# Optimization experiments

Hardware: AMD Instinct MI355X
Metric: run time of the kernel (lower is better)

Reference implementation:

```python
import jax, jax.numpy as jnp
import numpy as np

B, S, H = 2, 2048, 2048
NH, NKV, HD = 16, 4, 128
GROUPS = NH // NKV
THETA = 10000.0
EPS = 1e-6


def setup_inputs() -> dict:
    key = jax.random.key(0)
    ks = jax.random.split(key, 6)
    scale = 0.02
    return {
        "hidden_states": jax.random.normal(ks[0], (B, S, H), jnp.float32),
        "wq": jax.random.normal(ks[1], (NH * HD, H), jnp.float32) * scale,
        "wk": jax.random.normal(ks[2], (NKV * HD, H), jnp.float32) * scale,
        "wv": jax.random.normal(ks[3], (NKV * HD, H), jnp.float32) * scale,
        "wo": jax.random.normal(ks[4], (H, NH * HD), jnp.float32) * scale,
        "q_norm_weight": jnp.ones((HD,), jnp.float32),
        "k_norm_weight": jnp.ones((HD,), jnp.float32),
    }


def _rope_tables(seq_len):
    inv_freq = 1.0 / (THETA ** (jnp.arange(0, HD, 2, dtype=jnp.float32) / HD))
    t = jnp.arange(seq_len, dtype=jnp.float32)
    freqs = jnp.outer(t, inv_freq)              # [S, HD/2]
    emb = jnp.concatenate([freqs, freqs], -1)   # [S, HD]
    return jnp.cos(emb), jnp.sin(emb)


def _rotate_half(x):
    x1, x2 = x[..., : HD // 2], x[..., HD // 2:]
    return jnp.concatenate([-x2, x1], -1)


def _rmsnorm(x, w):
    var = jnp.mean(jnp.square(x), axis=-1, keepdims=True)
    return x * jax.lax.rsqrt(var + EPS) * w


def reference(hidden_states, wq, wk, wv, wo, q_norm_weight, k_norm_weight):
    b, s, _ = hidden_states.shape
    q = (hidden_states @ wq.T).reshape(b, s, NH, HD).transpose(0, 2, 1, 3)    # [b,nh,s,d]
    k = (hidden_states @ wk.T).reshape(b, s, NKV, HD).transpose(0, 2, 1, 3)   # [b,nkv,s,d]
    v = (hidden_states @ wv.T).reshape(b, s, NKV, HD).transpose(0, 2, 1, 3)

    cos, sin = _rope_tables(s)                  # [s,d]
    q = q * cos + _rotate_half(q) * sin
    k = k * cos + _rotate_half(k) * sin

    # fused QK RMSNorm (applied inside fused_qknorm_flash_attention)
    q = _rmsnorm(q, q_norm_weight)
    k = _rmsnorm(k, k_norm_weight)

    # GQA: share each kv head across GROUPS query heads without materializing repeats
    qg = q.reshape(b, NKV, GROUPS, s, HD)
    scale = 1.0 / jnp.sqrt(jnp.float32(HD))
    scores = jnp.einsum('bhgqd,bhkd->bhgqk', qg, k) * scale   # [b,nkv,g,s,s]
    causal = jnp.tril(jnp.ones((s, s), bool))
    scores = jnp.where(causal, scores, jnp.finfo(scores.dtype).min)
    probs = jax.nn.softmax(scores, axis=-1)
    out = jnp.einsum('bhgqk,bhkd->bhgqd', probs, v)            # [b,nkv,g,s,d]
    out = out.reshape(b, NH, s, HD).transpose(0, 2, 1, 3).reshape(b, s, NH * HD)
    return out @ wo.T
```

## Files before the change

kernel.cpp:

```cpp
#include <hip/hip_runtime.h>
#include <math.h>

typedef __bf16 bf16;
typedef __bf16 bf16x8 __attribute__((ext_vector_type(8)));
typedef __bf16 bf16x4 __attribute__((ext_vector_type(4)));
typedef float f32x4 __attribute__((ext_vector_type(4)));
typedef unsigned int u32;

#define B_DIM 2
#define S_LEN 2048
#define H_DIM 2048
#define NH 16
#define NKV 4
#define HD 128

__device__ __forceinline__ void gl_lds16(const void* g, void* l) {
    __builtin_amdgcn_global_load_lds(
        (const __attribute__((address_space(1))) unsigned int*)g,
        (__attribute__((address_space(3))) unsigned int*)l, 16, 0, 0);
}

__device__ __forceinline__ void bar() {
    asm volatile("" ::: "memory");
    __builtin_amdgcn_s_barrier();
    asm volatile("" ::: "memory");
}

__global__ __launch_bounds__(256) void cast_all(const float* __restrict__ s0,
                                                const float* __restrict__ s1,
                                                const float* __restrict__ s2,
                                                const float* __restrict__ s3,
                                                const float* __restrict__ s4,
                                                bf16* __restrict__ dst) {
    const int i = blockIdx.x * 256 + threadIdx.x;
    const float* src;
    int off;
    if (i < 2097152)      { src = s0; off = 0; }
    else if (i < 3145728) { src = s1; off = 2097152; }
    else if (i < 3407872) { src = s2; off = 3145728; }
    else if (i < 3670016) { src = s3; off = 3407872; }
    else                  { src = s4; off = 3670016; }
    float4 f = ((const float4*)src)[i - off];
    bf16x4 o = { (bf16)f.x, (bf16)f.y, (bf16)f.z, (bf16)f.w };
    *(bf16x4*)(dst + (size_t)i * 4) = o;
}

template <typename OutT>
__global__ __launch_bounds__(512, 2) void gemm256(const bf16* __restrict__ A,
                                                  const bf16* __restrict__ Bt,
                                                  OutT* __restrict__ C,
                                                  int M, int N, int K) {
    __shared__ __align__(16) bf16 smem[65536];
    const int t = threadIdx.x, lane = t & 63, w = t >> 6;
    const int lr = lane & 15, quad = lane >> 4;
    const int nN = N >> 8;
    const int nwg = gridDim.x, chunk = nwg >> 3;
    const int bid = blockIdx.x;
    const int lid = (bid & 7) * chunk + (bid >> 3);
    const int m0 = (lid / nN) << 8, n0 = (lid % nN) << 8;
    const int mh_w = w >> 2;
    const int wn = (w & 3) << 6;
    const int nh_w = (w & 3) >> 1;
    const int rb = (w & 1) << 6;
    const int nK = K >> 6;

    const int ld0 = w * 2;
    const int lrow = lane >> 2;
    const int csrc = (lane & 3) ^ ((lane >> 3) & 3);
    const int swz = (lr >> 1) & 3;

    auto stA = [&](int ts, int mh) {
        if (ts < nK) {
            bf16* db = smem + (ts & 1) * 16384 + mh * 8192;
            const bf16* sp = A + (size_t)(m0 + mh * 128) * K + ts * 64;
#pragma unroll
            for (int i = 0; i < 2; i++) {
                const int ldi = ld0 + i, kb = ldi >> 3, rg = ldi & 7;
                gl_lds16(sp + (size_t)(rg * 16 + lrow) * K + kb * 32 + csrc * 8,
                         db + kb * 4096 + rg * 512);
            }
        }
    };
    auto stB = [&](int ts, int nh) {
        if (ts < nK) {
            bf16* db = smem + 32768 + (ts & 1) * 16384 + nh * 8192;
            const bf16* sp = Bt + (size_t)(n0 + nh * 128) * K + ts * 64;
#pragma unroll
            for (int i = 0; i < 2; i++) {
                const int ldi = ld0 + i, kb = ldi >> 3, rg = ldi & 7;
                gl_lds16(sp + (size_t)(rg * 16 + lrow) * K + kb * 32 + csrc * 8,
                         db + kb * 4096 + rg * 512);
            }
        }
    };

    f32x4 acc[8][4];
#pragma unroll
    for (int i = 0; i < 8; i++)
#pragma unroll
        for (int j = 0; j < 4; j++) acc[i][j] = (f32x4){0.f, 0.f, 0.f, 0.f};
    bf16x8 af[8], b0[4], b1[4];

    auto rdA = [&](int s, int fi0) {
        const bf16* bp = smem + s * 16384 + mh_w * 8192;
#pragma unroll
        for (int f = 0; f < 4; f++)
#pragma unroll
            for (int ks = 0; ks < 2; ks++)
                af[f * 2 + ks] = *(const bf16x8*)(bp + ks * 4096 +
                                                  ((fi0 + f) * 16 + lr) * 32 + (quad ^ swz) * 8);
    };
    auto rdB = [&](int s, int fj0, bf16x8* dst) {
        const bf16* bp = smem + 32768 + s * 16384 + nh_w * 8192;
#pragma unroll
        for (int f = 0; f < 2; f++)
#pragma unroll
            for (int ks = 0; ks < 2; ks++)
                dst[f * 2 + ks] = *(const bf16x8*)(bp + ks * 4096 +
                                                   (rb + (fj0 + f) * 16 + lr) * 32 + (quad ^ swz) * 8);
    };
    auto mm16 = [&](int fi0, int fj0, bf16x8* bb) {
        __builtin_amdgcn_s_setprio(1);
#pragma unroll
        for (int f = 0; f < 4; f++)
#pragma unroll
            for (int g = 0; g < 2; g++)
#pragma unroll
                for (int ks = 0; ks < 2; ks++)
                    acc[fi0 + f][fj0 + g] = __builtin_amdgcn_mfma_f32_16x16x32_bf16(
                        af[f * 2 + ks], bb[g * 2 + ks], acc[fi0 + f][fj0 + g], 0, 0, 0);
        __builtin_amdgcn_s_setprio(0);
    };

    stA(0, 0); stA(0, 1); stB(0, 0); stB(0, 1); stA(1, 0);
    asm volatile("s_waitcnt vmcnt(2)" ::: "memory");
    bar();

    for (int ts = 0; ts < nK; ++ts) {
        const int s = ts & 1;
        rdA(s, 0); rdB(s, 0, b0);
        stA(ts + 1, 1);
        bar();
        mm16(0, 0, b0);
        bar();
        rdB(s, 2, b1);
        stB(ts + 1, 0);
        bar();
        mm16(0, 2, b1);
        bar();
        rdA(s, 4);
        stB(ts + 1, 1);
        bar();
        mm16(4, 2, b1);
        bar();
        rdB(s, 0, b0);
        stA(ts + 2, 0);
        bar();
        mm16(4, 0, b0);
        if (ts + 2 < nK) asm volatile("s_waitcnt vmcnt(2)" ::: "memory");
        else             asm volatile("s_waitcnt vmcnt(0)" ::: "memory");
        bar();
    }
#pragma unroll
    for (int fi = 0; fi < 8; fi++) {
        const int m = m0 + mh_w * 128 + fi * 16 + quad * 4;
#pragma unroll
        for (int fj = 0; fj < 4; fj++) {
            const int n = n0 + wn + fj * 16 + lr;
#pragma unroll
            for (int r = 0; r < 4; r++)
                C[(size_t)(m + r) * N + n] = (OutT)acc[fi][fj][r];
        }
    }
}

__global__ __launch_bounds__(512, 1) void gemm_pn(const bf16* __restrict__ A,
                                                  const bf16* __restrict__ Bt,
                                                  float* __restrict__ C,
                                                  int M, int N, int K) {
    __shared__ __align__(16) bf16 smem[49152];
    const int t = threadIdx.x, lane = t & 63, w = t >> 6;
    const int lr = lane & 15, quad = lane >> 4;
    const int nN = N >> 7;
    const int nwg = gridDim.x, chunk = nwg >> 3;
    const int bid = blockIdx.x;
    const int lid = (bid & 7) * chunk + (bid >> 3);
    const int m0 = (lid / nN) << 8, n0 = (lid % nN) << 7;
    const int mh_w = w >> 2;
    const int wn = (w & 3) << 5;
    const int nK = K >> 6;

    const int ld0 = w * 2;
    const int lrow = lane >> 2;
    const int csrc = (lane & 3) ^ ((lane >> 3) & 3);
    const int swz = (lr >> 1) & 3;

    auto stA = [&](int ts, int mh) {
        if (ts < nK) {
            bf16* db = smem + (ts & 1) * 16384 + mh * 8192;
            const bf16* sp = A + (size_t)(m0 + mh * 128) * K + ts * 64;
#pragma unroll
            for (int i = 0; i < 2; i++) {
                const int ldi = ld0 + i, kb = ldi >> 3, rg = ldi & 7;
                gl_lds16(sp + (size_t)(rg * 16 + lrow) * K + kb * 32 + csrc * 8,
                         db + kb * 4096 + rg * 512);
            }
        }
    };
    auto stB1 = [&](int ts) {
        if (ts < nK) {
            bf16* db = smem + 32768 + (ts & 1) * 8192;
            const bf16* sp = Bt + (size_t)n0 * K + ts * 64;
#pragma unroll
            for (int i = 0; i < 2; i++) {
                const int ldi = ld0 + i, kb = ldi >> 3, rg = ldi & 7;
                gl_lds16(sp + (size_t)(rg * 16 + lrow) * K + kb * 32 + csrc * 8,
                         db + kb * 4096 + rg * 512);
            }
        }
    };

    f32x4 acc[8][2];
#pragma unroll
    for (int i = 0; i < 8; i++)
#pragma unroll
        for (int j = 0; j < 2; j++) acc[i][j] = (f32x4){0.f, 0.f, 0.f, 0.f};
    bf16x8 af[8], bf1[4];

    auto rdA = [&](int s, int fi0) {
        const bf16* bp = smem + s * 16384 + mh_w * 8192;
#pragma unroll
        for (int f = 0; f < 4; f++)
#pragma unroll
            for (int ks = 0; ks < 2; ks++)
                af[f * 2 + ks] = *(const bf16x8*)(bp + ks * 4096 +
                                                  ((fi0 + f) * 16 + lr) * 32 + (quad ^ swz) * 8);
    };
    auto rdB1 = [&](int s) {
        const bf16* bp = smem + 32768 + s * 8192;
#pragma unroll
        for (int f = 0; f < 2; f++)
#pragma unroll
            for (int ks = 0; ks < 2; ks++)
                bf1[f * 2 + ks] = *(const bf16x8*)(bp + ks * 4096 +
                                                   (wn + f * 16 + lr) * 32 + (quad ^ swz) * 8);
    };
    auto mm8 = [&](int fi0, int ks) {
        __builtin_amdgcn_s_setprio(1);
#pragma unroll
        for (int f = 0; f < 4; f++)
#pragma unroll
            for (int g = 0; g < 2; g++)
                acc[fi0 + f][g] = __builtin_amdgcn_mfma_f32_16x16x32_bf16(
                    af[f * 2 + ks], bf1[g * 2 + ks], acc[fi0 + f][g], 0, 0, 0);
        __builtin_amdgcn_s_setprio(0);
    };

    stA(0, 0); stA(0, 1); stB1(0);
    asm volatile("s_waitcnt vmcnt(0)" ::: "memory");
    bar();

    for (int ts = 0; ts < nK; ++ts) {
        const int s = ts & 1;
        rdA(s, 0); rdB1(s);
        stA(ts + 1, 0);
        bar();
        mm8(0, 0);
        bar();
        stA(ts + 1, 1);
        stB1(ts + 1);
        bar();
        mm8(0, 1);
        bar();
        rdA(s, 4);
        bar();
        mm8(4, 0);
        bar();
        mm8(4, 1);
        asm volatile("s_waitcnt vmcnt(0)" ::: "memory");
        bar();
    }
#pragma unroll
    for (int fi = 0; fi < 8; fi++) {
        const int m = m0 + mh_w * 128 + fi * 16 + quad * 4;
#pragma unroll
        for (int fj = 0; fj < 2; fj++) {
            const int n = n0 + wn + fj * 16 + lr;
#pragma unroll
            for (int r = 0; r < 4; r++)
                C[(size_t)(m + r) * N + n] = acc[fi][fj][r];
        }
    }
}

__global__ __launch_bounds__(256) void rope_rms(const bf16* __restrict__ qkv,
                                                const float* __restrict__ qw,
                                                const float* __restrict__ kw,
                                                bf16* __restrict__ qb,
                                                bf16* __restrict__ kb,
                                                bf16* __restrict__ vt) {
    const int tok = blockIdx.x;
    const int b = tok >> 11, s = tok & (S_LEN - 1);
    const int lane = threadIdx.x & 63, w = threadIdx.x >> 6;
    const bf16* row = qkv + (size_t)tok * 3072;
    const float inv = expf(-(float)lane * (9.210340371976184f / 64.f));
    const float ang = (float)s * inv;
    float s_, c_;
    sincosf(ang, &s_, &c_);
    const float wq1 = qw[lane], wq2 = qw[lane + 64];
    const float wk1 = kw[lane], wk2 = kw[lane + 64];
    for (int u = w; u < 24; u += 4) {
        if (u < 16) {
            const float x1 = (float)row[u * 128 + lane], x2 = (float)row[u * 128 + 64 + lane];
            float y1 = x1 * c_ - x2 * s_;
            float y2 = x2 * c_ + x1 * s_;
            float ss = y1 * y1 + y2 * y2;
#pragma unroll
            for (int m = 1; m < 64; m <<= 1) ss += __shfl_xor(ss, m);
            const float r = rsqrtf(ss * (1.f / 128.f) + 1e-6f);
            size_t o = ((size_t)(b * NH + u) * S_LEN + s) * HD;
            qb[o + lane]      = (bf16)(y1 * r * wq1);
            qb[o + 64 + lane] = (bf16)(y2 * r * wq2);
        } else if (u < 20) {
            const int kh = u - 16;
            const float x1 = (float)row[2048 + kh * 128 + lane], x2 = (float)row[2048 + kh * 128 + 64 + lane];
            float y1 = x1 * c_ - x2 * s_;
            float y2 = x2 * c_ + x1 * s_;
            float ss = y1 * y1 + y2 * y2;
#pragma unroll
            for (int m = 1; m < 64; m <<= 1) ss += __shfl_xor(ss, m);
            const float r = rsqrtf(ss * (1.f / 128.f) + 1e-6f);
            size_t base = (size_t)(b * NKV + kh) * 16 * 16384;
            kb[base + (size_t)(lane >> 3) * 16384 + s * 8 + (lane & 7)]       = (bf16)(y1 * r * wk1);
            kb[base + (size_t)(8 + (lane >> 3)) * 16384 + s * 8 + (lane & 7)] = (bf16)(y2 * r * wk2);
        } else {
            const int vh = u - 20;
            const float x1 = (float)row[2560 + vh * 128 + lane], x2 = (float)row[2560 + vh * 128 + 64 + lane];
            const int m = s & 31;
            const int gi = (s >> 5) * 4 + ((m & 15) >> 2);
            const int el = ((m >> 4) << 2) | (m & 3);
            size_t base = ((size_t)(b * NKV + vh) * 256 + gi) * 1024 + el;
            vt[base + (size_t)lane * 8]        = (bf16)x1;
            vt[base + (size_t)(lane + 64) * 8] = (bf16)x2;
        }
    }
}

__global__ __launch_bounds__(512, 4) void flash(const bf16* __restrict__ qg,
                                                const bf16* __restrict__ kg,
                                                const bf16* __restrict__ vg,
                                                bf16* __restrict__ attn,
                                                float* __restrict__ part_o,
                                                float* __restrict__ part_l) {
    static const unsigned char QT[22] = {9,8,15,15,7,14,14,13,13,6,12,12,11,11,5,10,10,4,3,2,1,0};
    static const unsigned char CK[22] = {2,2,0,1,2,0,1,0,1,2,0,1,0,1,2,0,1,2,2,2,2,2};
    const int idx = blockIdx.x;
    const int g = idx >> 5, hb = idx & 31;
    const int qt = QT[g], ck = CK[g];
    const int h = hb & 15, b = hb >> 4;
    const int kvh = h >> 2;
    const int ktBeg = (ck == 1) ? (qt + 1) : 0;
    const int ktEnd = (ck == 0) ? (qt + 1) : (2 * qt + 2);
    const bf16* qh = qg + (size_t)(b * NH + h) * S_LEN * HD;
    const bf16* kh = kg + (size_t)(b * NKV + kvh) * (16 * 16384);
    const bf16* vh = vg + (size_t)(b * NKV + kvh) * (256 * 1024);
    __shared__ __align__(16) bf16 Ks[2][16 * 512];
    __shared__ __align__(16) bf16 Vs[2][8 * 1024];
    const int t = threadIdx.x, lane = t & 63, w = t >> 6, lr = lane & 15, quad = lane >> 4;
    const int row0 = qt * 128 + w * 16;
    bf16x8 qf[4];
#pragma unroll
    for (int c = 0; c < 4; c++)
        qf[c] = *(const bf16x8*)(qh + (size_t)(row0 + lr) * HD + c * 32 + quad * 8);
    f32x4 o[8];
    f32x4 lacc = (f32x4){0.f, 0.f, 0.f, 0.f};
#pragma unroll
    for (int j = 0; j < 8; j++) o[j] = (f32x4){0.f, 0.f, 0.f, 0.f};
    const bf16 one = (bf16)1.0f;
    const bf16x8 ones8 = {one, one, one, one, one, one, one, one};
    const float C1 = 0.12751744f;
    const float C2 = -17.3123405f;

    const bf16* kp[2];
#pragma unroll
    for (int i = 0; i < 2; i++) kp[i] = kh + (size_t)(w * 2 + i) * 16384 + lane * 8;
    const bf16* vp = vh + (size_t)w * 1024 + lane * 8;

    auto stage = [&](int kt_, int bi) {
        const size_t kb8 = (size_t)kt_ * 512;
#pragma unroll
        for (int i = 0; i < 2; i++)
            gl_lds16(kp[i] + kb8, &Ks[bi][(w * 2 + i) * 512]);
        const size_t vb = (size_t)kt_ * 8192;
        gl_lds16(vp + vb, &Vs[bi][w * 1024]);
        gl_lds16(vp + vb + 512, &Vs[bi][w * 1024 + 512]);
    };

    stage(ktBeg, 0);
    __syncthreads();
    int cur = 0;

    for (int kt = ktBeg; kt < ktEnd; ++kt) {
        const int kbase = kt * 64;
        if (kt + 1 < ktEnd) stage(kt + 1, cur ^ 1);
        f32x4 sacc[4];
#pragma unroll
        for (int n = 0; n < 4; n++) sacc[n] = (f32x4){0.f, 0.f, 0.f, 0.f};
        __builtin_amdgcn_s_setprio(1);
#pragma unroll
        for (int c = 0; c < 4; c++)
#pragma unroll
            for (int n = 0; n < 4; n++) {
                bf16x8 kf = *(const bf16x8*)&Ks[cur][(c * 4 + quad) * 512 + (n * 16 + lr) * 8];
                sacc[n] = __builtin_amdgcn_mfma_f32_16x16x32_bf16(kf, qf[c], sacc[n], 0, 0, 0);
            }
        __builtin_amdgcn_s_setprio(0);
        const bool diag = (kt >= 2 * qt);
        u32 pw[8];
        {
            const int qrow = row0 + lr;
#pragma unroll
            for (int n = 0; n < 4; n++) {
                float e0, e1, e2, e3;
                {
                    float ev0 = exp2f(fmaf(sacc[n][0], C1, C2));
                    float ev1 = exp2f(fmaf(sacc[n][1], C1, C2));
                    float ev2 = exp2f(fmaf(sacc[n][2], C1, C2));
                    float ev3 = exp2f(fmaf(sacc[n][3], C1, C2));
                    if (diag) {
                        const int key = kbase + n * 16 + quad * 4;
                        ev0 = (key + 0 <= qrow) ? ev0 : 0.f;
                        ev1 = (key + 1 <= qrow) ? ev1 : 0.f;
                        ev2 = (key + 2 <= qrow) ? ev2 : 0.f;
                        ev3 = (key + 3 <= qrow) ? ev3 : 0.f;
                    }
                    e0 = ev0; e1 = ev1; e2 = ev2; e3 = ev3;
                }
                asm("v_cvt_pk_bf16_f32 %0, %1, %2"
                    : "=v"(pw[(n >> 1) * 4 + (n & 1) * 2 + 0]) : "v"(e0), "v"(e1));
                asm("v_cvt_pk_bf16_f32 %0, %1, %2"
                    : "=v"(pw[(n >> 1) * 4 + (n & 1) * 2 + 1]) : "v"(e2), "v"(e3));
            }
        }
        __builtin_amdgcn_s_setprio(1);
#pragma unroll
        for (int k2 = 0; k2 < 2; k2++) {
            const bf16x8 p0 = *(const bf16x8*)&pw[k2 * 4];
#pragma unroll
            for (int j = 0; j < 8; j++) {
                bf16x8 vf = *(const bf16x8*)&Vs[cur][(k2 * 4 + quad) * 1024 + (j * 16 + lr) * 8];
                o[j] = __builtin_amdgcn_mfma_f32_16x16x32_bf16(vf, p0, o[j], 0, 0, 0);
            }
            lacc = __builtin_amdgcn_mfma_f32_16x16x32_bf16(ones8, p0, lacc, 0, 0, 0);
        }
        __builtin_amdgcn_s_setprio(0);
        __syncthreads();
        cur ^= 1;
    }
    if (ck == 2) {
        const float inv = 1.0f / lacc[0];
        const int qrow = row0 + lr;
        bf16* dst = attn + ((size_t)(b * S_LEN) + qrow) * (NH * HD) + h * HD + quad * 4;
#pragma unroll
        for (int j = 0; j < 8; j++) {
            bf16x4 st = { (bf16)(o[j][0] * inv), (bf16)(o[j][1] * inv),
                          (bf16)(o[j][2] * inv), (bf16)(o[j][3] * inv) };
            *(bf16x4*)(dst + j * 16) = st;
        }
    } else {
        const int slot = ((b * NH + h) * 6 + (qt - 10)) * 2 + ck;
        float* po = part_o + (size_t)slot * 16384;
        const int row = w * 16 + lr;
#pragma unroll
        for (int j = 0; j < 8; j++) {
            float4 st = { o[j][0], o[j][1], o[j][2], o[j][3] };
            *(float4*)(po + row * 128 + j * 16 + quad * 4) = st;
        }
        if (quad == 0) part_l[slot * 128 + row] = lacc[0];
    }
}

__global__ __launch_bounds__(256) void reduce_attn(const float* __restrict__ part_o,
                                                   const float* __restrict__ part_l,
                                                   bf16* __restrict__ attn) {
    const int blk = blockIdx.x;
    const int qt = (blk % 6) + 10;
    const int h = (blk / 6) & 15, b = blk / 96;
    const float* p0 = part_o + (size_t)(blk * 2 + 0) * 16384;
    const float* p1 = part_o + (size_t)(blk * 2 + 1) * 16384;
    const float* l0 = part_l + (blk * 2 + 0) * 128;
    const float* l1 = part_l + (blk * 2 + 1) * 128;
    const int t = threadIdx.x;
#pragma unroll
    for (int it = 0; it < 16; it++) {
        const int idx = it * 256 + t;
        const int row = idx >> 5, d4 = idx & 31;
        float4 a = ((const float4*)p0)[idx];
        float4 c = ((const float4*)p1)[idx];
        const float inv = 1.0f / (l0[row] + l1[row]);
        bf16x4 ov = { (bf16)((a.x + c.x) * inv), (bf16)((a.y + c.y) * inv),
                      (bf16)((a.z + c.z) * inv), (bf16)((a.w + c.w) * inv) };
        *(bf16x4*)(attn + ((size_t)(b * S_LEN) + qt * 128 + row) * (NH * HD) + h * HD + d4 * 4) = ov;
    }
}

extern "C" void kernel_launch(void* const* d_in, const int* in_sizes, int n_in,
                              void* d_out, int out_size, void* d_ws, size_t ws_size,
                              hipStream_t stream) {
    (void)in_sizes; (void)n_in; (void)out_size; (void)ws_size;
    const float* hs  = (const float*)d_in[0];
    const float* wq  = (const float*)d_in[1];
    const float* wk  = (const float*)d_in[2];
    const float* wv  = (const float*)d_in[3];
    const float* wo  = (const float*)d_in[4];
    const float* qnw = (const float*)d_in[5];
    const float* knw = (const float*)d_in[6];
    float* out = (float*)d_out;

    char* ws = (char*)d_ws;
    size_t off = 0;
    auto alloc = [&](size_t bytes) {
        void* p = ws + off;
        off += (bytes + 255) & ~(size_t)255;
        return p;
    };
    bf16* hs_bf   = (bf16*)alloc((size_t)4096 * 2048 * 2);
    bf16* wqkv_bf = (bf16*)alloc((size_t)3072 * 2048 * 2);
    bf16* wo_bf   = (bf16*)alloc((size_t)2048 * 2048 * 2);
    bf16* qkv_bf  = (bf16*)alloc((size_t)4096 * 3072 * 2);
    bf16* q_bf    = (bf16*)alloc((size_t)B_DIM * NH * S_LEN * HD * 2);
    bf16* k_bf    = (bf16*)alloc((size_t)B_DIM * NKV * S_LEN * HD * 2);
    bf16* vt_bf   = (bf16*)alloc((size_t)B_DIM * NKV * S_LEN * HD * 2);
    bf16* at_bf   = (bf16*)alloc((size_t)4096 * 2048 * 2);

    float* part_o = (float*)hs_bf;
    float* part_l = (float*)((char*)hs_bf + (size_t)384 * 16384 * 4);

    cast_all<<<18432, 256, 0, stream>>>(hs, wq, wk, wv, wo, hs_bf);
    gemm256<bf16><<<dim3(192), 512, 0, stream>>>(hs_bf, wqkv_bf, qkv_bf, 4096, 3072, 2048);
    rope_rms<<<4096, 256, 0, stream>>>(qkv_bf, qnw, knw, q_bf, k_bf, vt_bf);
    flash<<<dim3(704), 512, 0, stream>>>(q_bf, k_bf, vt_bf, at_bf, part_o, part_l);
    reduce_attn<<<dim3(192), 256, 0, stream>>>(part_o, part_l, at_bf);
    gemm_pn<<<dim3(256), 512, 0, stream>>>(at_bf, wo_bf, out, 4096, 2048, 2048);
}
```

Baseline: 303.3 us.

## Retile QKV projection GEMM to 256x192 tiles for full CU occupancy

Replaces the generic 256x256 GEMM for the QKV projection with a specialized 256x192-tile kernel, raising the grid from 192 to 256 workgroups so every CU on the device gets work and the wave-quantization tail is reduced. The B-tile LDS layout, the load schedule and the fragment reads are restructured into three 64-row subtiles, with each wave covering 48 columns. The cost is lower arithmetic intensity per tile and irregular 2+1 fragment handling, which could reduce MFMA efficiency.

```diff
diff --git a/kernel.cpp b/kernel.cpp
--- a/kernel.cpp
+++ b/kernel.cpp
@@ -45,23 +45,20 @@
     *(bf16x4*)(dst + (size_t)i * 4) = o;
 }
 
-template <typename OutT>
-__global__ __launch_bounds__(512, 2) void gemm256(const bf16* __restrict__ A,
-                                                  const bf16* __restrict__ Bt,
-                                                  OutT* __restrict__ C,
-                                                  int M, int N, int K) {
-    __shared__ __align__(16) bf16 smem[65536];
+__global__ __launch_bounds__(512, 2) void gemm_qkv(const bf16* __restrict__ A,
+                                                   const bf16* __restrict__ Bt,
+                                                   bf16* __restrict__ C,
+                                                   int M, int N, int K) {
+    __shared__ __align__(16) bf16 smem[57344];
     const int t = threadIdx.x, lane = t & 63, w = t >> 6;
     const int lr = lane & 15, quad = lane >> 4;
-    const int nN = N >> 8;
+    const int nN = N / 192;
     const int nwg = gridDim.x, chunk = nwg >> 3;
     const int bid = blockIdx.x;
     const int lid = (bid & 7) * chunk + (bid >> 3);
-    const int m0 = (lid / nN) << 8, n0 = (lid % nN) << 8;
+    const int m0 = (lid / nN) << 8, n0 = (lid % nN) * 192;
     const int mh_w = w >> 2;
-    const int wn = (w & 3) << 6;
-    const int nh_w = (w & 3) >> 1;
-    const int rb = (w & 1) << 6;
+    const int wn = (w & 3) * 48;
     const int nK = K >> 6;
 
     const int ld0 = w * 2;
@@ -81,25 +78,21 @@
             }
         }
     };
-    auto stB = [&](int ts, int nh) {
+    auto stB = [&](int ts, int sub) {
         if (ts < nK) {
-            bf16* db = smem + 32768 + (ts & 1) * 16384 + nh * 8192;
-            const bf16* sp = Bt + (size_t)(n0 + nh * 128) * K + ts * 64;
-#pragma unroll
-            for (int i = 0; i < 2; i++) {
-                const int ldi = ld0 + i, kb = ldi >> 3, rg = ldi & 7;
-                gl_lds16(sp + (size_t)(rg * 16 + lrow) * K + kb * 32 + csrc * 8,
-                         db + kb * 4096 + rg * 512);
-            }
-        }
-    };
-
-    f32x4 acc[8][4];
+            bf16* db = smem + 32768 + (ts & 1) * 12288 + sub * 4096 +
+                       (w >> 2) * 2048 + (w & 3) * 512;
+            const bf16* sp = Bt + (size_t)(n0 + sub * 64) * K + ts * 64;
+            gl_lds16(sp + (size_t)((w & 3) * 16 + lrow) * K + (w >> 2) * 32 + csrc * 8, db);
+        }
+    };
+
+    f32x4 acc[8][3];
 #pragma unroll
     for (int i = 0; i < 8; i++)
 #pragma unroll
-        for (int j = 0; j < 4; j++) acc[i][j] = (f32x4){0.f, 0.f, 0.f, 0.f};
-    bf16x8 af[8], b0[4], b1[4];
+        for (int j = 0; j < 3; j++) acc[i][j] = (f32x4){0.f, 0.f, 0.f, 0.f};
+    bf16x8 af[8], b0[4], b1[2];
 
     auto rdA = [&](int s, int fi0) {
         const bf16* bp = smem + s * 16384 + mh_w * 8192;
@@ -110,53 +103,59 @@
                 af[f * 2 + ks] = *(const bf16x8*)(bp + ks * 4096 +
                                                   ((fi0 + f) * 16 + lr) * 32 + (quad ^ swz) * 8);
     };
-    auto rdB = [&](int s, int fj0, bf16x8* dst) {
-        const bf16* bp = smem + 32768 + s * 16384 + nh_w * 8192;
-#pragma unroll
-        for (int f = 0; f < 2; f++)
+    auto rdB = [&](int s, int fj0, int nf, bf16x8* dst) {
+        const bf16* bp = smem + 32768 + s * 12288;
+#pragma unroll
+        for (int f = 0; f < 2; f++) {
+            if (f >= nf) break;
+            const int rowb = wn + (fj0 + f) * 16;
+            const int sub = rowb >> 6, r64 = rowb & 63;
 #pragma unroll
             for (int ks = 0; ks < 2; ks++)
-                dst[f * 2 + ks] = *(const bf16x8*)(bp + ks * 4096 +
-                                                   (rb + (fj0 + f) * 16 + lr) * 32 + (quad ^ swz) * 8);
-    };
-    auto mm16 = [&](int fi0, int fj0, bf16x8* bb) {
+                dst[f * 2 + ks] = *(const bf16x8*)(bp + sub * 4096 + ks * 2048 +
+                                                   (r64 + lr) * 32 + (quad ^ swz) * 8);
+        }
+    };
+    auto mmq = [&](int fi0, int fj0, int nf, bf16x8* bb) {
         __builtin_amdgcn_s_setprio(1);
 #pragma unroll
         for (int f = 0; f < 4; f++)
 #pragma unroll
-            for (int g = 0; g < 2; g++)
+            for (int g = 0; g < 2; g++) {
+                if (g >= nf) break;
 #pragma unroll
                 for (int ks = 0; ks < 2; ks++)
                     acc[fi0 + f][fj0 + g] = __builtin_amdgcn_mfma_f32_16x16x32_bf16(
                         af[f * 2 + ks], bb[g * 2 + ks], acc[fi0 + f][fj0 + g], 0, 0, 0);
+            }
         __builtin_amdgcn_s_setprio(0);
     };
 
-    stA(0, 0); stA(0, 1); stB(0, 0); stB(0, 1); stA(1, 0);
+    stA(0, 0); stA(0, 1); stB(0, 0); stB(0, 1); stB(0, 2); stA(1, 0);
     asm volatile("s_waitcnt vmcnt(2)" ::: "memory");
     bar();
 
     for (int ts = 0; ts < nK; ++ts) {
         const int s = ts & 1;
-        rdA(s, 0); rdB(s, 0, b0);
+        rdA(s, 0); rdB(s, 0, 2, b0);
         stA(ts + 1, 1);
         bar();
-        mm16(0, 0, b0);
-        bar();
-        rdB(s, 2, b1);
-        stB(ts + 1, 0);
-        bar();
-        mm16(0, 2, b1);
+        mmq(0, 0, 2, b0);
+        bar();
+        rdB(s, 2, 1, b1);
+        stB(ts + 1, 0); stB(ts + 1, 1);
+        bar();
+        mmq(0, 2, 1, b1);
         bar();
         rdA(s, 4);
-        stB(ts + 1, 1);
-        bar();
-        mm16(4, 2, b1);
-        bar();
-        rdB(s, 0, b0);
+        stB(ts + 1, 2);
+        bar();
+        mmq(4, 2, 1, b1);
+        bar();
+        rdB(s, 0, 2, b0);
         stA(ts + 2, 0);
         bar();
-        mm16(4, 0, b0);
+        mmq(4, 0, 2, b0);
         if (ts + 2 < nK) asm volatile("s_waitcnt vmcnt(2)" ::: "memory");
         else             asm volatile("s_waitcnt vmcnt(0)" ::: "memory");
         bar();
@@ -165,11 +164,11 @@
     for (int fi = 0; fi < 8; fi++) {
         const int m = m0 + mh_w * 128 + fi * 16 + quad * 4;
 #pragma unroll
-        for (int fj = 0; fj < 4; fj++) {
+        for (int fj = 0; fj < 3; fj++) {
             const int n = n0 + wn + fj * 16 + lr;
 #pragma unroll
             for (int r = 0; r < 4; r++)
-                C[(size_t)(m + r) * N + n] = (OutT)acc[fi][fj][r];
+                C[(size_t)(m + r) * N + n] = (bf16)acc[fi][fj][r];
         }
     }
 }
@@ -537,7 +536,7 @@
     float* part_l = (float*)((char*)hs_bf + (size_t)384 * 16384 * 4);
 
     cast_all<<<18432, 256, 0, stream>>>(hs, wq, wk, wv, wo, hs_bf);
-    gemm256<bf16><<<dim3(192), 512, 0, stream>>>(hs_bf, wqkv_bf, qkv_bf, 4096, 3072, 2048);
+    gemm_qkv<<<dim3(256), 512, 0, stream>>>(hs_bf, wqkv_bf, qkv_bf, 4096, 3072, 2048);
     rope_rms<<<4096, 256, 0, stream>>>(qkv_bf, qnw, knw, q_bf, k_bf, vt_bf);
     flash<<<dim3(704), 512, 0, stream>>>(q_bf, k_bf, vt_bf, at_bf, part_o, part_l);
     reduce_attn<<<dim3(192), 256, 0, stream>>>(part_o, part_l, at_bf);
```

Measured after the change: 295.4 us. 2.6% less time.
